# Kernel optimization log

Measured on AMD Instinct MI355X. Metric: run time of the kernel, lower is better.

Reference implementation:

```python
import jax, jax.numpy as jnp
import numpy as np

N_NODES = 50000
N_EDGES = 800000
N_GRAPHS = 64
FEAT = 128
HID = 256
ACT = 32


def setup_inputs() -> dict:
    key = jax.random.key(0)
    ks = jax.random.split(key, 16)
    x = jax.random.normal(ks[0], (N_NODES, FEAT), dtype=jnp.float32)
    edge_index = jax.random.randint(ks[1], (2, N_EDGES), 0, N_NODES, dtype=jnp.int32)
    # sorted graph assignment covering all graphs (avoids empty segments in mean pool)
    batch = (jnp.arange(N_NODES, dtype=jnp.int32) * N_GRAPHS) // N_NODES
    action = jax.random.normal(ks[2], (N_GRAPHS, ACT), dtype=jnp.float32)

    def lin(k, fan_in, fan_out):
        s = 1.0 / np.sqrt(fan_in)
        kw, kb = jax.random.split(k)
        W = jax.random.uniform(kw, (fan_in, fan_out), jnp.float32, -s, s)
        b = jax.random.uniform(kb, (fan_out,), jnp.float32, -s, s)
        return W, b

    q1_W1, q1_b1 = lin(ks[3], FEAT, HID)
    q1_W2, q1_b2 = lin(ks[4], HID, HID)
    q1_fcW, q1_fcb = lin(ks[5], HID + ACT, 1)
    q2_W1, q2_b1 = lin(ks[6], FEAT, HID)
    q2_W2, q2_b2 = lin(ks[7], HID, HID)
    q2_fcW, q2_fcb = lin(ks[8], HID + ACT, 1)
    return dict(x=x, edge_index=edge_index, batch=batch, action=action,
                q1_W1=q1_W1, q1_b1=q1_b1, q1_W2=q1_W2, q1_b2=q1_b2,
                q1_fcW=q1_fcW, q1_fcb=q1_fcb,
                q2_W1=q2_W1, q2_b1=q2_b1, q2_W2=q2_W2, q2_b2=q2_b2,
                q2_fcW=q2_fcW, q2_fcb=q2_fcb)


def _gcn_conv(x, W, b, src, dst, norm, n_nodes):
    # GCNConv: h = D^-1/2 (A+I) D^-1/2 (x W) + b
    h = x @ W                                    # [N, out]
    msg = h[src] * norm[:, None]                 # [E+N, out] gather
    out = jax.ops.segment_sum(msg, dst, num_segments=n_nodes)  # scatter-add
    return out + b


def _critic_head(x, src, dst, norm, batch, action, W1, b1, W2, b2, fcW, fcb, counts):
    n = x.shape[0]
    h = jax.nn.relu(_gcn_conv(x, W1, b1, src, dst, norm, n))
    h = jax.nn.relu(_gcn_conv(h, W2, b2, src, dst, norm, n))
    pooled = jax.ops.segment_sum(h, batch, num_segments=N_GRAPHS) / counts[:, None]
    q_in = jnp.concatenate([pooled, action], axis=-1)
    return q_in @ fcW + fcb


def reference(x, edge_index, batch, action,
              q1_W1, q1_b1, q1_W2, q1_b2, q1_fcW, q1_fcb,
              q2_W1, q2_b1, q2_W2, q2_b2, q2_fcW, q2_fcb):
    n = x.shape[0]
    # add self-loops (PyG GCNConv default)
    loops = jnp.arange(n, dtype=edge_index.dtype)
    src = jnp.concatenate([edge_index[0], loops])
    dst = jnp.concatenate([edge_index[1], loops])
    deg = jax.ops.segment_sum(jnp.ones_like(dst, x.dtype), dst, num_segments=n)
    dis = jnp.where(deg > 0, jax.lax.rsqrt(deg), 0.0)
    norm = dis[src] * dis[dst]                   # symmetric normalization per edge
    counts = jax.ops.segment_sum(jnp.ones_like(batch, x.dtype), batch,
                                 num_segments=N_GRAPHS)
    q1 = _critic_head(x, src, dst, norm, batch, action,
                      q1_W1, q1_b1, q1_W2, q1_b2, q1_fcW, q1_fcb, counts)
    q2 = _critic_head(x, src, dst, norm, batch, action,
                      q2_W1, q2_b1, q2_W2, q2_b2, q2_fcW, q2_fcb, counts)
    return (q1, q2)
```

## Files before the change

### kernel.cpp

```cpp
#include <hip/hip_runtime.h>
#include <hip/hip_bf16.h>

#define FEAT 128
#define HID  256
#define ACTD 32

typedef __attribute__((ext_vector_type(8))) short bf16x8;
typedef __attribute__((ext_vector_type(4))) float f32x4;
typedef __attribute__((ext_vector_type(2))) float f32x2;

__device__ __forceinline__ ushort f2b(float f) {
    __hip_bfloat16 h = __float2bfloat16(f);
    return *(ushort*)&h;
}
__device__ __forceinline__ uint pack2(float lo, float hi) {
    return (uint)f2b(lo) | ((uint)f2b(hi) << 16);
}
__device__ __forceinline__ f32x2 upk_lo(uint u) { return __builtin_amdgcn_cvt_pk_f32_fp8(u, false); }
__device__ __forceinline__ f32x2 upk_hi(uint u) { return __builtin_amdgcn_cvt_pk_f32_fp8(u, true); }

__device__ __forceinline__ void add8(float* acc, uint2 g) {
    f32x2 l0 = upk_lo(g.x), h0 = upk_hi(g.x);
    f32x2 l1 = upk_lo(g.y), h1 = upk_hi(g.y);
    acc[0] += l0[0]; acc[1] += l0[1]; acc[2] += h0[0]; acc[3] += h0[1];
    acc[4] += l1[0]; acc[5] += l1[1]; acc[6] += h1[0]; acc[7] += h1[1];
}


__global__ void hist_bounds(const int* __restrict__ dst, int* __restrict__ cnt, int E,
                            const int* __restrict__ batch, int* __restrict__ sg,
                            int* __restrict__ eg, int n) {
    int i = blockIdx.x * blockDim.x + threadIdx.x;
    if (i < E) atomicAdd(&cnt[dst[i]], 1);
    if (i < n) {
        int b = batch[i];
        if (i == 0 || batch[i - 1] != b) sg[b] = i;
        if (i == n - 1 || batch[i + 1] != b) eg[b] = i + 1;
    }
}

__global__ __launch_bounds__(256) void scan_local(const int* __restrict__ cnt,
        int* __restrict__ local, int* __restrict__ bsum, int n) {
    __shared__ int s[256];
    int t = threadIdx.x;
    int i = blockIdx.x * 256 + t;
    int v = (i < n) ? cnt[i] : 0;
    s[t] = v;
    __syncthreads();
    for (int off = 1; off < 256; off <<= 1) {
        int u = (t >= off) ? s[t - off] : 0;
        __syncthreads();
        s[t] += u;
        __syncthreads();
    }
    if (i < n) local[i] = s[t];
    if (t == 255) bsum[blockIdx.x] = s[255];
}

__global__ __launch_bounds__(256) void scan_bsum(int* __restrict__ bsum, int nb) {
    __shared__ int s[256];
    int t = threadIdx.x;
    s[t] = (t < nb) ? bsum[t] : 0;
    __syncthreads();
    for (int off = 1; off < 256; off <<= 1) {
        int u = (t >= off) ? s[t - off] : 0;
        __syncthreads();
        s[t] += u;
        __syncthreads();
    }
    if (t < nb) bsum[t] = (t == 0) ? 0 : s[t - 1];
}

__global__ __launch_bounds__(256) void scan_finish(const int* __restrict__ local,
        const int* __restrict__ bsum, const int* __restrict__ cnt,
        int* __restrict__ row_ptr, int* __restrict__ fill_pos,
        float* __restrict__ dis, int n) {
    int i = blockIdx.x * 256 + threadIdx.x;
    if (i >= n) return;
    int c = cnt[i];
    int inc = local[i] + bsum[blockIdx.x];
    int ex = inc - c;
    row_ptr[i] = ex;
    fill_pos[i] = ex;
    dis[i] = rsqrtf((float)c + 1.0f);
    if (i == n - 1) row_ptr[n] = inc;
}

__global__ void fill_kernel(const int* __restrict__ src, const int* __restrict__ dst,
        int* __restrict__ fill_pos, int* __restrict__ col_idx, int E) {
    int e = blockIdx.x * blockDim.x + threadIdx.x;
    if (e < E) {
        int d = dst[e];
        int pos = atomicAdd(&fill_pos[d], 1);
        col_idx[pos] = src[e];
    }
}

__global__ void prep_ws(const float* __restrict__ x, const float* __restrict__ dis,
                        uchar* __restrict__ xs,
                        const float* __restrict__ W1a, const float* __restrict__ W1b,
                        const float* __restrict__ W2a, const float* __restrict__ W2b,
                        ushort* __restrict__ WT1, uchar* __restrict__ WT2f, int n) {
    int i = blockIdx.x * blockDim.x + threadIdx.x;
    const int nscale = n * (FEAT / 4);
    if (i < nscale) {
        int v = i >> 5;
        float dv = dis[v] * 8.f;
        float4 f = ((const float4*)x)[i];
        uint p = __builtin_amdgcn_cvt_pk_fp8_f32(f.x * dv, f.y * dv, 0, false);
        p = __builtin_amdgcn_cvt_pk_fp8_f32(f.z * dv, f.w * dv, p, true);
        ((uint*)xs)[i] = p;
        return;
    }
    i -= nscale;
    if (i < 2 * FEAT * HID) {
        int head = i >> 15;
        int rem = i & 32767;
        int k = rem >> 8, nn = rem & 255;
        const float* W = head ? W1b : W1a;
        WT1[(size_t)(head * 256 + nn) * FEAT + k] = f2b(W[rem]);
    } else {
        int j = i - 2 * FEAT * HID;
        if (j >= 2 * HID * HID) return;
        int head = j >> 16;
        int rem = j & 65535;
        int k = rem >> 8, nn = rem & 255;
        const float* W = head ? W2b : W2a;
        float v = W[rem] * 8.f;
        uint q = __builtin_amdgcn_cvt_pk_fp8_f32(v, v, 0, false);
        WT2f[(size_t)head * 65536 + nn * 256 + k] = (uchar)(q & 0xff);
    }
}


__global__ __launch_bounds__(256) void agg128(
        const uchar* __restrict__ xs, const float* __restrict__ dis,
        const int* __restrict__ row_ptr, const int* __restrict__ col_idx,
        ushort* __restrict__ z, int n) {
    const int wave = threadIdx.x >> 6, lane = threadIdx.x & 63;
    const int v = blockIdx.x * 4 + wave;
    if (v >= n) return;
    const ushort* X = (const ushort*)xs;
    f32x2 p = upk_lo((uint)X[(size_t)v * 64 + lane]);
    float a0 = p[0], a1 = p[1];
    const int e0 = row_ptr[v], e1 = row_ptr[v + 1];
    int e = e0;
    for (; e + 8 <= e1; e += 8) {
        uint m[8];
#pragma unroll
        for (int j = 0; j < 8; ++j) m[j] = X[(size_t)col_idx[e + j] * 64 + lane];
#pragma unroll
        for (int j = 0; j < 8; ++j) {
            f32x2 q = upk_lo(m[j]);
            a0 += q[0]; a1 += q[1];
        }
    }
    for (; e < e1; ++e) {
        f32x2 m = upk_lo((uint)X[(size_t)col_idx[e] * 64 + lane]);
        a0 += m[0]; a1 += m[1];
    }
    float sc = dis[v] * 0.125f;
    ((uint*)z)[(size_t)v * 64 + lane] = pack2(a0 * sc, a1 * sc);
}


__global__ __launch_bounds__(256) void agg512(
        const uchar* __restrict__ h1, const float* __restrict__ dis,
        const int* __restrict__ row_ptr, const int* __restrict__ col_idx,
        uchar* __restrict__ z2f, int n) {
    const int wave = threadIdx.x >> 6, lane = threadIdx.x & 63;
    const int v = blockIdx.x * 4 + wave;
    if (v >= n) return;
    const uint2* H = (const uint2*)h1;
    float acc[8];
    {
        uint2 g = H[(size_t)v * 64 + lane];
        f32x2 l0 = upk_lo(g.x), h0 = upk_hi(g.x);
        f32x2 l1 = upk_lo(g.y), h1v = upk_hi(g.y);
        acc[0] = l0[0]; acc[1] = l0[1]; acc[2] = h0[0]; acc[3] = h0[1];
        acc[4] = l1[0]; acc[5] = l1[1]; acc[6] = h1v[0]; acc[7] = h1v[1];
    }
    const int e0 = row_ptr[v], e1 = row_ptr[v + 1];
    int e = e0;
    for (; e + 8 <= e1; e += 8) {
        uint2 m[8];
#pragma unroll
        for (int j = 0; j < 8; ++j) m[j] = H[(size_t)col_idx[e + j] * 64 + lane];
#pragma unroll
        for (int j = 0; j < 8; ++j) add8(acc, m[j]);
    }
    for (; e < e1; ++e) add8(acc, H[(size_t)col_idx[e] * 64 + lane]);
    float sc = dis[v] * 0.25f;
    uint lo = __builtin_amdgcn_cvt_pk_fp8_f32(acc[0] * sc, acc[1] * sc, 0, false);
    lo = __builtin_amdgcn_cvt_pk_fp8_f32(acc[2] * sc, acc[3] * sc, lo, true);
    uint hi = __builtin_amdgcn_cvt_pk_fp8_f32(acc[4] * sc, acc[5] * sc, 0, false);
    hi = __builtin_amdgcn_cvt_pk_fp8_f32(acc[6] * sc, acc[7] * sc, hi, true);
    uint2 o = {lo, hi};
    ((uint2*)z2f)[(size_t)v * 64 + lane] = o;
}


__global__ __launch_bounds__(512) void gemm1_mfma(
        const ushort* __restrict__ z,
        const ushort* __restrict__ WT1,
        const float* __restrict__ b1a, const float* __restrict__ b1b,
        const float* __restrict__ dis,
        uchar* __restrict__ out, int M) {
    constexpr int K = FEAT;
    __shared__ char Bs[256 * 256];
    const int tid = threadIdx.x;
    const int bm = blockIdx.x * 128;
    const int head = blockIdx.y;
    const ushort* WT = WT1 + (size_t)head * 256 * K;
    const float* bias = head ? b1b : b1a;

    for (int idx = tid; idx < 256 * 16; idx += 512) {
        int nr = idx >> 4, seg = idx & 15;
        int4 val = *(const int4*)(WT + (size_t)nr * K + seg * 8);
        int byte = (nr * 256 + seg * 16) ^ ((nr & 7) << 4);
        *(int4*)(Bs + byte) = val;
    }
    __syncthreads();

    const int warp = tid >> 6, lane = tid & 63;
    const int wr = warp >> 1, wc = warp & 1;
    const int kgrp = lane >> 4;
    const int r0 = wr * 32 + (lane & 15);
    const int c0 = wc * 128 + (lane & 15);

    f32x4 acc[2][8] = {};
    const bf16x8 zv = {};
    for (int ks = 0; ks < 4; ++ks) {
        bf16x8 a[2], b[8];
#pragma unroll
        for (int m = 0; m < 2; ++m) {
            int grow = bm + r0 + m * 16;
            a[m] = (grow < M)
                 ? *(const bf16x8*)(z + (size_t)grow * K + ks * 32 + kgrp * 8)
                 : zv;
        }
#pragma unroll
        for (int nf = 0; nf < 8; ++nf) {
            int nr = c0 + nf * 16;
            int byte = (nr * 256 + ks * 64 + kgrp * 16) ^ ((nr & 7) << 4);
            b[nf] = *(const bf16x8*)(Bs + byte);
        }
#pragma unroll
        for (int nf = 0; nf < 8; ++nf)
#pragma unroll
            for (int m = 0; m < 2; ++m)
                acc[m][nf] = __builtin_amdgcn_mfma_f32_16x16x32_bf16(b[nf], a[m], acc[m][nf], 0, 0, 0);
    }

    const int ml = lane & 15;
    const int ngrp = (lane >> 4) * 4;
#pragma unroll
    for (int m = 0; m < 2; ++m) {
        int grow = bm + wr * 32 + m * 16 + ml;
        if (grow >= M) continue;
        float d = dis[grow] * 16.f;
#pragma unroll
        for (int nf = 0; nf < 8; ++nf) {
            int n0 = wc * 128 + nf * 16 + ngrp;
            float4 bv = *(const float4*)(bias + n0);
            f32x4 ac = acc[m][nf];
            float v0 = fmaxf(ac[0] + bv.x, 0.f) * d;
            float v1 = fmaxf(ac[1] + bv.y, 0.f) * d;
            float v2 = fmaxf(ac[2] + bv.z, 0.f) * d;
            float v3 = fmaxf(ac[3] + bv.w, 0.f) * d;
            uint q = __builtin_amdgcn_cvt_pk_fp8_f32(v0, v1, 0, false);
            q = __builtin_amdgcn_cvt_pk_fp8_f32(v2, v3, q, true);
            *(uint*)(out + (size_t)grow * 512 + head * 256 + n0) = q;
        }
    }
}


__global__ __launch_bounds__(512) void gemm2_pool(
        const uchar* __restrict__ z2f,
        const uchar* __restrict__ WT2f,
        const float* __restrict__ b2a, const float* __restrict__ b2b,
        const int* __restrict__ batch,
        float* __restrict__ pooled, int M) {
    constexpr int K = HID;
    __shared__ char Bs[256 * 256];
    __shared__ int rows_g[128];
    const int tid = threadIdx.x;
    const int bm = blockIdx.x * 128;
    const int head = blockIdx.y;
    const uchar* WT = WT2f + (size_t)head * 65536;
    const float* bias = head ? b2b : b2a;

    for (int idx = tid; idx < 256 * 32; idx += 512) {
        int nr = idx >> 5, seg = idx & 31;
        uint2 val = *(const uint2*)(WT + (size_t)nr * 256 + seg * 8);
        int byte = (nr * 256 + seg * 8) ^ ((nr & 7) << 3);
        *(uint2*)(Bs + byte) = val;
    }
    if (tid < 128) rows_g[tid] = batch[min(bm + tid, M - 1)];
    __syncthreads();

    const int warp = tid >> 6, lane = tid & 63;
    const int wr = warp >> 1, wc = warp & 1;
    const int kgrp = lane >> 4;
    const int r0 = wr * 32 + (lane & 15);
    const int c0 = wc * 128 + (lane & 15);
    const uchar* Abase = z2f + (size_t)head * 256;

    f32x4 acc[2][8] = {};
    for (int ks = 0; ks < 8; ++ks) {
        long a[2], b[8];
#pragma unroll
        for (int m = 0; m < 2; ++m) {
            int grow = bm + r0 + m * 16;
            a[m] = (grow < M)
                 ? *(const long*)(Abase + (size_t)grow * 512 + ks * 32 + kgrp * 8)
                 : 0L;
        }
#pragma unroll
        for (int nf = 0; nf < 8; ++nf) {
            int nr = c0 + nf * 16;
            int byte = (nr * 256 + ks * 32 + kgrp * 8) ^ ((nr & 7) << 3);
            b[nf] = *(const long*)(Bs + byte);
        }
#pragma unroll
        for (int nf = 0; nf < 8; ++nf)
#pragma unroll
            for (int m = 0; m < 2; ++m)
                acc[m][nf] = __builtin_amdgcn_mfma_f32_16x16x32_fp8_fp8(a[m], b[nf], acc[m][nf], 0, 0, 0);
    }

    const int rbw = wr * 32;
    const int g0 = rows_g[rbw];
    const int glast = rows_g[min(127, rbw + 31)];
    float s0[8] = {}, s1[8] = {};
#pragma unroll
    for (int m = 0; m < 2; ++m) {
#pragma unroll
        for (int r = 0; r < 4; ++r) {
            int lrow = rbw + m * 16 + (lane >> 4) * 4 + r;
            int grow = bm + lrow;
            if (grow < M) {
                bool in0 = (rows_g[lrow] == g0);
#pragma unroll
                for (int nf = 0; nf < 8; ++nf) {
                    float val = fmaxf(acc[m][nf][r] * 0.03125f + bias[c0 + nf * 16], 0.f);
                    if (in0) s0[nf] += val; else s1[nf] += val;
                }
            }
        }
    }
#pragma unroll
    for (int nf = 0; nf < 8; ++nf) {
        s0[nf] += __shfl_xor(s0[nf], 16, 64);
        s0[nf] += __shfl_xor(s0[nf], 32, 64);
        s1[nf] += __shfl_xor(s1[nf], 16, 64);
        s1[nf] += __shfl_xor(s1[nf], 32, 64);
    }
    if (kgrp == 0) {
#pragma unroll
        for (int nf = 0; nf < 8; ++nf) {
            int n = head * 256 + c0 + nf * 16;
            atomicAdd(&pooled[(size_t)g0 * 512 + n], s0[nf]);
            if (glast != g0) atomicAdd(&pooled[(size_t)glast * 512 + n], s1[nf]);
        }
    }
}

__global__ __launch_bounds__(512) void final_dot(
        const float* __restrict__ pooled, const int* __restrict__ sg,
        const int* __restrict__ eg, const float* __restrict__ action,
        const float* __restrict__ fcW1, const float* __restrict__ fcb1,
        const float* __restrict__ fcW2, const float* __restrict__ fcb2,
        float* __restrict__ out, int G) {
    int g = blockIdx.x, t = threadIdx.x;
    int head = t >> 8, f = t & 255;
    const float* fcW = head ? fcW2 : fcW1;
    float inv = 1.f / (float)(eg[g] - sg[g]);
    float p = pooled[g * 512 + t] * inv * fcW[f];
    if (f < ACTD) p += action[g * ACTD + f] * fcW[HID + f];
    for (int off = 32; off; off >>= 1) p += __shfl_down(p, off, 64);
    __shared__ float red[8];
    if ((t & 63) == 0) red[t >> 6] = p;
    __syncthreads();
    if (t == 0)   out[g]     = red[0] + red[1] + red[2] + red[3] + fcb1[0];
    if (t == 256) out[G + g] = red[4] + red[5] + red[6] + red[7] + fcb2[0];
}


extern "C" void kernel_launch(void* const* d_in, const int* in_sizes, int n_in,
                              void* d_out, int out_size, void* d_ws, size_t ws_size,
                              hipStream_t stream) {
    const float* x      = (const float*)d_in[0];
    const int*   ei     = (const int*)d_in[1];
    const int*   batch  = (const int*)d_in[2];
    const float* action = (const float*)d_in[3];
    const float* q1_W1  = (const float*)d_in[4];
    const float* q1_b1  = (const float*)d_in[5];
    const float* q1_W2  = (const float*)d_in[6];
    const float* q1_b2  = (const float*)d_in[7];
    const float* q1_fcW = (const float*)d_in[8];
    const float* q1_fcb = (const float*)d_in[9];
    const float* q2_W1  = (const float*)d_in[10];
    const float* q2_b1  = (const float*)d_in[11];
    const float* q2_W2  = (const float*)d_in[12];
    const float* q2_b2  = (const float*)d_in[13];
    const float* q2_fcW = (const float*)d_in[14];
    const float* q2_fcb = (const float*)d_in[15];

    const int N = in_sizes[2];
    const int E = in_sizes[1] / 2;
    const int G = in_sizes[3] / ACTD;
    const int* src = ei;
    const int* dst = ei + E;

    char* w = (char*)d_ws;
    size_t off = 0;
    auto take = [&](size_t bytes) -> void* {
        void* p = w + off;
        off = (off + bytes + 255) & ~(size_t)255;
        return p;
    };
    int*    cnt      = (int*)take((size_t)(N + 1) * 4);
    int*    row_ptr  = (int*)take((size_t)(N + 1) * 4);
    int*    fill_pos = (int*)take((size_t)N * 4);
    int*    slocal   = (int*)take((size_t)N * 4);
    int*    bsum     = (int*)take((size_t)256 * 4);
    float*  dis      = (float*)take((size_t)N * 4);
    int*    col_idx  = (int*)take((size_t)E * 4);
    int*    sg       = (int*)take((size_t)G * 4);
    int*    eg       = (int*)take((size_t)G * 4);
    ushort* WT1      = (ushort*)take((size_t)512 * FEAT * 2);
    uchar*  WT2f     = (uchar*)take((size_t)2 * HID * HID);
    float*  pooled   = (float*)take((size_t)G * 512 * 4);
    uchar*  xs       = (uchar*)take((size_t)N * FEAT);
    ushort* z        = (ushort*)take((size_t)N * FEAT * 2);
    uchar*  h1       = (uchar*)take((size_t)N * 512);
    uchar*  z2f      = (uchar*)take((size_t)N * 512);
    (void)ws_size;

    const int TB = 256;
    const int nb = (N + 255) / 256;
    hipMemsetAsync(cnt, 0, (size_t)(N + 1) * 4, stream);
    hipMemsetAsync(pooled, 0, (size_t)G * 512 * 4, stream);

    int hb_grid = (max(E, N) + TB - 1) / TB;
    hist_bounds<<<hb_grid, TB, 0, stream>>>(dst, cnt, E, batch, sg, eg, N);
    scan_local<<<nb, TB, 0, stream>>>(cnt, slocal, bsum, N);
    scan_bsum<<<1, TB, 0, stream>>>(bsum, nb);
    scan_finish<<<nb, TB, 0, stream>>>(slocal, bsum, cnt, row_ptr, fill_pos, dis, N);
    fill_kernel<<<(E + TB - 1) / TB, TB, 0, stream>>>(src, dst, fill_pos, col_idx, E);

    int ptotal = N * (FEAT / 4) + 2 * FEAT * HID + 2 * HID * HID;
    prep_ws<<<(ptotal + TB - 1) / TB, TB, 0, stream>>>(x, dis, xs,
                                                       q1_W1, q2_W1, q1_W2, q2_W2,
                                                       WT1, WT2f, N);

    int agg_grid = (N + 3) / 4;
    int gx128 = (N + 127) / 128;

    agg128<<<agg_grid, TB, 0, stream>>>(xs, dis, row_ptr, col_idx, z, N);
    gemm1_mfma<<<dim3(gx128, 2), 512, 0, stream>>>(z, WT1, q1_b1, q2_b1, dis, h1, N);
    agg512<<<agg_grid, TB, 0, stream>>>(h1, dis, row_ptr, col_idx, z2f, N);
    gemm2_pool<<<dim3(gx128, 2), 512, 0, stream>>>(z2f, WT2f, q1_b2, q2_b2, batch,
                                                   pooled, N);
    final_dot<<<G, 512, 0, stream>>>(pooled, sg, eg, action,
                                     q1_fcW, q1_fcb, q2_fcW, q2_fcb,
                                     (float*)d_out, G);
}
```

Baseline: 278.5 us.

## Replace three-pass scan with atomic-ticket scan and fuse fill with prep

The three scan kernels become one, where each block claims its base offset with an atomicAdd on a ticket counter, so CSR segments are laid out in arbitrary block order and stored as separate start and end arrays. The edge fill kernel is merged into the prep kernel's launch, removing several launches and the intermediate scan buffers. This trades ordered, contiguous row layout for fewer kernel launches. Segments may also be less contiguous, which can slightly change gather locality.

```diff
diff --git a/kernel.cpp b/kernel.cpp
--- a/kernel.cpp
+++ b/kernel.cpp
@@ -39,13 +39,16 @@
     }
 }
 
-__global__ __launch_bounds__(256) void scan_local(const int* __restrict__ cnt,
-        int* __restrict__ local, int* __restrict__ bsum, int n) {
+__global__ __launch_bounds__(256) void scan_one(const int* __restrict__ cnt,
+        int* __restrict__ row_ptr, int* __restrict__ row_end,
+        int* __restrict__ fill_pos, float* __restrict__ dis,
+        int* __restrict__ ticket, int n) {
     __shared__ int s[256];
+    __shared__ int base_sh;
     int t = threadIdx.x;
     int i = blockIdx.x * 256 + t;
-    int v = (i < n) ? cnt[i] : 0;
-    s[t] = v;
+    int c = (i < n) ? cnt[i] : 0;
+    s[t] = c;
     __syncthreads();
     for (int off = 1; off < 256; off <<= 1) {
         int u = (t >= off) ? s[t - off] : 0;
@@ -53,55 +56,32 @@
         s[t] += u;
         __syncthreads();
     }
-    if (i < n) local[i] = s[t];
-    if (t == 255) bsum[blockIdx.x] = s[255];
-}
-
-__global__ __launch_bounds__(256) void scan_bsum(int* __restrict__ bsum, int nb) {
-    __shared__ int s[256];
-    int t = threadIdx.x;
-    s[t] = (t < nb) ? bsum[t] : 0;
+    if (t == 255) base_sh = atomicAdd(ticket, s[255]);
     __syncthreads();
-    for (int off = 1; off < 256; off <<= 1) {
-        int u = (t >= off) ? s[t - off] : 0;
-        __syncthreads();
-        s[t] += u;
-        __syncthreads();
-    }
-    if (t < nb) bsum[t] = (t == 0) ? 0 : s[t - 1];
-}
-
-__global__ __launch_bounds__(256) void scan_finish(const int* __restrict__ local,
-        const int* __restrict__ bsum, const int* __restrict__ cnt,
-        int* __restrict__ row_ptr, int* __restrict__ fill_pos,
-        float* __restrict__ dis, int n) {
-    int i = blockIdx.x * 256 + threadIdx.x;
-    if (i >= n) return;
-    int c = cnt[i];
-    int inc = local[i] + bsum[blockIdx.x];
-    int ex = inc - c;
-    row_ptr[i] = ex;
-    fill_pos[i] = ex;
-    dis[i] = rsqrtf((float)c + 1.0f);
-    if (i == n - 1) row_ptr[n] = inc;
-}
-
-__global__ void fill_kernel(const int* __restrict__ src, const int* __restrict__ dst,
-        int* __restrict__ fill_pos, int* __restrict__ col_idx, int E) {
-    int e = blockIdx.x * blockDim.x + threadIdx.x;
-    if (e < E) {
-        int d = dst[e];
+    if (i < n) {
+        int ex = base_sh + s[t] - c;
+        row_ptr[i] = ex;
+        row_end[i] = ex + c;
+        fill_pos[i] = ex;
+        dis[i] = rsqrtf((float)c + 1.0f);
+    }
+}
+
+__global__ void fill_prep(const int* __restrict__ src, const int* __restrict__ dst,
+                          int* __restrict__ fill_pos, int* __restrict__ col_idx, int E,
+                          const float* __restrict__ x, const float* __restrict__ dis,
+                          uchar* __restrict__ xs,
+                          const float* __restrict__ W1a, const float* __restrict__ W1b,
+                          const float* __restrict__ W2a, const float* __restrict__ W2b,
+                          ushort* __restrict__ WT1, uchar* __restrict__ WT2f, int n) {
+    int i = blockIdx.x * blockDim.x + threadIdx.x;
+    if (i < E) {
+        int d = dst[i];
         int pos = atomicAdd(&fill_pos[d], 1);
-        col_idx[pos] = src[e];
-    }
-}
-
-__global__ void prep_ws(const float* __restrict__ x, const float* __restrict__ dis,
-                        uchar* __restrict__ xs,
-                        const float* __restrict__ W1a, const float* __restrict__ W1b,
-                        const float* __restrict__ W2a, const float* __restrict__ W2b,
-                        ushort* __restrict__ WT1, uchar* __restrict__ WT2f, int n) {
-    int i = blockIdx.x * blockDim.x + threadIdx.x;
+        col_idx[pos] = src[i];
+        return;
+    }
+    i -= E;
     const int nscale = n * (FEAT / 4);
     if (i < nscale) {
         int v = i >> 5;
@@ -135,7 +115,8 @@
 
 __global__ __launch_bounds__(256) void agg128(
         const uchar* __restrict__ xs, const float* __restrict__ dis,
-        const int* __restrict__ row_ptr, const int* __restrict__ col_idx,
+        const int* __restrict__ row_ptr, const int* __restrict__ row_end,
+        const int* __restrict__ col_idx,
         ushort* __restrict__ z, int n) {
     const int wave = threadIdx.x >> 6, lane = threadIdx.x & 63;
     const int v = blockIdx.x * 4 + wave;
@@ -143,7 +124,7 @@
     const ushort* X = (const ushort*)xs;
     f32x2 p = upk_lo((uint)X[(size_t)v * 64 + lane]);
     float a0 = p[0], a1 = p[1];
-    const int e0 = row_ptr[v], e1 = row_ptr[v + 1];
+    const int e0 = row_ptr[v], e1 = row_end[v];
     int e = e0;
     for (; e + 8 <= e1; e += 8) {
         uint m[8];
@@ -166,7 +147,8 @@
 
 __global__ __launch_bounds__(256) void agg512(
         const uchar* __restrict__ h1, const float* __restrict__ dis,
-        const int* __restrict__ row_ptr, const int* __restrict__ col_idx,
+        const int* __restrict__ row_ptr, const int* __restrict__ row_end,
+        const int* __restrict__ col_idx,
         uchar* __restrict__ z2f, int n) {
     const int wave = threadIdx.x >> 6, lane = threadIdx.x & 63;
     const int v = blockIdx.x * 4 + wave;
@@ -180,7 +162,7 @@
         acc[0] = l0[0]; acc[1] = l0[1]; acc[2] = h0[0]; acc[3] = h0[1];
         acc[4] = l1[0]; acc[5] = l1[1]; acc[6] = h1v[0]; acc[7] = h1v[1];
     }
-    const int e0 = row_ptr[v], e1 = row_ptr[v + 1];
+    const int e0 = row_ptr[v], e1 = row_end[v];
     int e = e0;
     for (; e + 8 <= e1; e += 8) {
         uint2 m[8];
@@ -422,10 +404,9 @@
         return p;
     };
     int*    cnt      = (int*)take((size_t)(N + 1) * 4);
-    int*    row_ptr  = (int*)take((size_t)(N + 1) * 4);
+    int*    row_ptr  = (int*)take((size_t)N * 4);
+    int*    row_end  = (int*)take((size_t)N * 4);
     int*    fill_pos = (int*)take((size_t)N * 4);
-    int*    slocal   = (int*)take((size_t)N * 4);
-    int*    bsum     = (int*)take((size_t)256 * 4);
     float*  dis      = (float*)take((size_t)N * 4);
     int*    col_idx  = (int*)take((size_t)E * 4);
     int*    sg       = (int*)take((size_t)G * 4);
@@ -446,22 +427,19 @@
 
     int hb_grid = (max(E, N) + TB - 1) / TB;
     hist_bounds<<<hb_grid, TB, 0, stream>>>(dst, cnt, E, batch, sg, eg, N);
-    scan_local<<<nb, TB, 0, stream>>>(cnt, slocal, bsum, N);
-    scan_bsum<<<1, TB, 0, stream>>>(bsum, nb);
-    scan_finish<<<nb, TB, 0, stream>>>(slocal, bsum, cnt, row_ptr, fill_pos, dis, N);
-    fill_kernel<<<(E + TB - 1) / TB, TB, 0, stream>>>(src, dst, fill_pos, col_idx, E);
-
-    int ptotal = N * (FEAT / 4) + 2 * FEAT * HID + 2 * HID * HID;
-    prep_ws<<<(ptotal + TB - 1) / TB, TB, 0, stream>>>(x, dis, xs,
-                                                       q1_W1, q2_W1, q1_W2, q2_W2,
-                                                       WT1, WT2f, N);
+    scan_one<<<nb, TB, 0, stream>>>(cnt, row_ptr, row_end, fill_pos, dis, cnt + N, N);
+
+    int fptotal = E + N * (FEAT / 4) + 2 * FEAT * HID + 2 * HID * HID;
+    fill_prep<<<(fptotal + TB - 1) / TB, TB, 0, stream>>>(
+        src, dst, fill_pos, col_idx, E,
+        x, dis, xs, q1_W1, q2_W1, q1_W2, q2_W2, WT1, WT2f, N);
 
     int agg_grid = (N + 3) / 4;
     int gx128 = (N + 127) / 128;
 
-    agg128<<<agg_grid, TB, 0, stream>>>(xs, dis, row_ptr, col_idx, z, N);
+    agg128<<<agg_grid, TB, 0, stream>>>(xs, dis, row_ptr, row_end, col_idx, z, N);
     gemm1_mfma<<<dim3(gx128, 2), 512, 0, stream>>>(z, WT1, q1_b1, q2_b1, dis, h1, N);
-    agg512<<<agg_grid, TB, 0, stream>>>(h1, dis, row_ptr, col_idx, z2f, N);
+    agg512<<<agg_grid, TB, 0, stream>>>(h1, dis, row_ptr, row_end, col_idx, z2f, N);
     gemm2_pool<<<dim3(gx128, 2), 512, 0, stream>>>(z2f, WT2f, q1_b2, q2_b2, batch,
                                                    pooled, N);
     final_dot<<<G, 512, 0, stream>>>(pooled, sg, eg, action,
```

Result: faster. 269.1 us (-3.4%).
